# Kernel tuning notes

Measured on AMD Instinct MI355X. Metric: run time of the kernel, lower is better.

The kernel has to match this reference:

```python
import jax, jax.numpy as jnp
import numpy as np

N = 128            # cache entries selected per ray (init arg n)
M = 3 * N          # cache rows
B = 65536          # rays in batch
NUM_SAMPLES = 256  # total samples per ray; inner sampler supplies NUM_SAMPLES - N


def _unit(k, shape):
    v = jax.random.normal(k, shape, dtype=jnp.float32)
    return v / jnp.linalg.norm(v, axis=-1, keepdims=True)


def setup_inputs() -> dict:
    key = jax.random.key(0)
    k0, k1, k2, k3, k4, k5 = jax.random.split(key, 6)
    cache_dirs = _unit(k0, (M, 3))
    cache_mip = jax.random.uniform(k1, (M, 1), dtype=jnp.float32)
    cache_bright = jax.random.uniform(k2, (M, 1), dtype=jnp.float32)
    cache = jnp.concatenate([cache_dirs, cache_mip, cache_bright], axis=1)  # (M,5)
    refdirs = _unit(k3, (B, 3))
    normal = _unit(k4, (B, 3))
    samp_rays = _unit(k5, (B, NUM_SAMPLES - N, 3))
    samp_mipval = jax.random.uniform(jax.random.fold_in(k5, 1), (B, NUM_SAMPLES - N), dtype=jnp.float32)
    return {"cache": cache, "refdirs": refdirs, "normal": normal,
            "samp_rays": samp_rays, "samp_mipval": samp_mipval}


def reference(cache, refdirs, normal, samp_rays, samp_mipval):
    # BrightnessSampler.sample with cache_init=True (n = N cache rays appended).
    cache_dirs = cache[:, :3]      # (M,3)
    cache_mip = cache[:, 3]        # (M,)
    # hemisphere test and directional similarity against every cached ray
    hemi = jnp.einsum('bd,md->bm', normal, cache_dirs)    # (B,M)
    sim = jnp.einsum('bd,md->bm', refdirs, cache_dirs)    # (B,M)
    score = jnp.where(hemi > 0, -sim, jnp.float32(0.0))   # (B,M)
    # torch: inds = argsort(score, dim=1) < n ; boolean-mask gather in original
    # position order. Replicate: keep original positions j where order[b,j] < N.
    order = jnp.argsort(score, axis=1)                    # (B,M)
    mask = order < N
    pos = jnp.where(mask, jnp.arange(M)[None, :], M)
    sel_pos = jnp.sort(pos, axis=1)[:, :N]                # (B,N) ascending original positions
    sel_rays = cache_dirs[sel_pos]                        # (B,N,3)
    sel_mipval = cache_mip[sel_pos]                       # (B,N)
    rays = jnp.concatenate([samp_rays, sel_rays], axis=1)       # (B,NUM_SAMPLES,3)
    mipval = jnp.concatenate([samp_mipval, sel_mipval], axis=1)  # (B,NUM_SAMPLES)
    return rays, mipval
```

## Files before the change

kernel.cpp:

```cpp
#include <hip/hip_runtime.h>

#define NCACHE 384
#define NSEL   128

__device__ __forceinline__ unsigned int sortable_bits(float f) {
    unsigned int u = __float_as_uint(f);
    return (u & 0x80000000u) ? ~u : (u | 0x80000000u);
}

struct __align__(16) u64x2 { unsigned long long x, y; };

__global__ __launch_bounds__(256) void fused_kernel(
    const float*  __restrict__ cache,
    const float*  __restrict__ refdirs,
    const float*  __restrict__ normal,
    const float4* __restrict__ samp_rays4,
    const float4* __restrict__ samp_mip4,
    float* __restrict__ out, int B)
{
#pragma clang fp contract(off)
    __shared__ float sdx[NCACHE], sdy[NCACHE], sdz[NCACHE], smip[NCACHE];
    __shared__ __align__(16) unsigned long long keys[4][NCACHE];
    __shared__ unsigned int bitmap[4][12];

    const int tid  = threadIdx.x;
    const int wave = tid >> 6;
    const int lane = tid & 63;
    const int b    = blockIdx.x * 4 + wave;

    for (int m = tid; m < NCACHE; m += 256) {
        sdx[m]  = cache[m * 5 + 0];
        sdy[m]  = cache[m * 5 + 1];
        sdz[m]  = cache[m * 5 + 2];
        smip[m] = cache[m * 5 + 3];
    }
    if (tid < 48) (&bitmap[0][0])[tid] = 0u;

    const float nx = normal[b * 3 + 0], ny = normal[b * 3 + 1], nz = normal[b * 3 + 2];
    const float rx = refdirs[b * 3 + 0], ry = refdirs[b * 3 + 1], rz = refdirs[b * 3 + 2];

    __syncthreads();

    for (int m = lane; m < NCACHE; m += 64) {
        float dx = sdx[m], dy = sdy[m], dz = sdz[m];
        float hemi = __builtin_fmaf(nz, dz, __builtin_fmaf(ny, dy, nx * dx));
        float sim  = __builtin_fmaf(rz, dz, __builtin_fmaf(ry, dy, rx * dx));
        float val  = (hemi > 0.0f) ? -sim : 0.0f;
        val = val + 0.0f;
        keys[wave][m] = ((unsigned long long)sortable_bits(val) << 32) | (unsigned int)m;
    }
    __syncthreads();

    const unsigned long long k0 = keys[wave][lane];
    const unsigned long long k1 = keys[wave][lane + 64];
    const u64x2* kp = (const u64x2*)&keys[wave][0];
    int r0 = 0, r1 = 0;
#pragma unroll 8
    for (int j = 0; j < NCACHE / 2; ++j) {
        u64x2 kk = kp[j];
        r0 += (kk.x < k0) ? 1 : 0;
        r0 += (kk.y < k0) ? 1 : 0;
        r1 += (kk.x < k1) ? 1 : 0;
        r1 += (kk.y < k1) ? 1 : 0;
    }

    atomicOr(&bitmap[wave][r0 >> 5], 1u << (r0 & 31));
    atomicOr(&bitmap[wave][r1 >> 5], 1u << (r1 & 31));
    __syncthreads();

    float* out_rays = out;
    float* out_mip  = out + (size_t)B * 768;

    {
        const int wi = r0 >> 5;
        int s = __popc(bitmap[wave][wi] & ((1u << (r0 & 31)) - 1u));
        for (int w = 0; w < wi; ++w) s += __popc(bitmap[wave][w]);
        const size_t rb = (size_t)b * 768 + 384 + (size_t)s * 3;
        out_rays[rb + 0] = sdx[r0];
        out_rays[rb + 1] = sdy[r0];
        out_rays[rb + 2] = sdz[r0];
        out_mip[(size_t)b * 256 + 128 + s] = smip[r0];
    }
    {
        const int wi = r1 >> 5;
        int s = __popc(bitmap[wave][wi] & ((1u << (r1 & 31)) - 1u));
        for (int w = 0; w < wi; ++w) s += __popc(bitmap[wave][w]);
        const size_t rb = (size_t)b * 768 + 384 + (size_t)s * 3;
        out_rays[rb + 0] = sdx[r1];
        out_rays[rb + 1] = sdy[r1];
        out_rays[rb + 2] = sdz[r1];
        out_mip[(size_t)b * 256 + 128 + s] = smip[r1];
    }

    float4* out4     = (float4*)out;
    float4* out_mip4 = (float4*)(out + (size_t)B * 768);
    const int b0 = blockIdx.x * 4;
#pragma unroll
    for (int i = tid; i < 512; i += 256) {
        const int bw  = i >> 7;
        const int off = i & 127;
        const int bb  = b0 + bw;
        if (off < 96) {
            out4[(size_t)bb * 192 + off] = samp_rays4[(size_t)bb * 96 + off];
        } else {
            out_mip4[(size_t)bb * 64 + (off - 96)] = samp_mip4[(size_t)bb * 32 + (off - 96)];
        }
    }
}

extern "C" void kernel_launch(void* const* d_in, const int* in_sizes, int n_in,
                              void* d_out, int out_size, void* d_ws, size_t ws_size,
                              hipStream_t stream) {
    const float* cache       = (const float*)d_in[0];
    const float* refdirs     = (const float*)d_in[1];
    const float* normal      = (const float*)d_in[2];
    const float* samp_rays   = (const float*)d_in[3];
    const float* samp_mipval = (const float*)d_in[4];
    float* out = (float*)d_out;

    const int B = in_sizes[1] / 3;

    fused_kernel<<<B / 4, 256, 0, stream>>>(cache, refdirs, normal,
                                            (const float4*)samp_rays,
                                            (const float4*)samp_mipval,
                                            out, B);
}
```

Measured before the change: 208.7 us.

## Compute ranks with wave ballots over register-held keys instead of LDS scan

Keys for all 384 cache entries are now kept in registers (six per lane) rather than written to LDS. Each candidate key is broadcast with readlane, and its rank is counted with six ballots and popcounts across the wave, which removes the LDS key array and one block barrier. The cost is 128 serial broadcast iterations of scalar and ballot work per wave, replacing per-lane streaming compares against 384 LDS keys, plus higher register pressure.

```diff
diff --git a/kernel.cpp b/kernel.cpp
--- a/kernel.cpp
+++ b/kernel.cpp
@@ -1,14 +1,11 @@
 #include <hip/hip_runtime.h>
 
 #define NCACHE 384
-#define NSEL   128
 
 __device__ __forceinline__ unsigned int sortable_bits(float f) {
     unsigned int u = __float_as_uint(f);
     return (u & 0x80000000u) ? ~u : (u | 0x80000000u);
 }
-
-struct __align__(16) u64x2 { unsigned long long x, y; };
 
 __global__ __launch_bounds__(256) void fused_kernel(
     const float*  __restrict__ cache,
@@ -20,7 +17,6 @@
 {
 #pragma clang fp contract(off)
     __shared__ float sdx[NCACHE], sdy[NCACHE], sdz[NCACHE], smip[NCACHE];
-    __shared__ __align__(16) unsigned long long keys[4][NCACHE];
     __shared__ unsigned int bitmap[4][12];
 
     const int tid  = threadIdx.x;
@@ -41,27 +37,35 @@
 
     __syncthreads();
 
-    for (int m = lane; m < NCACHE; m += 64) {
-        float dx = sdx[m], dy = sdy[m], dz = sdz[m];
+    unsigned long long k[6];
+#pragma unroll
+    for (int c = 0; c < 6; ++c) {
+        const int j = c * 64 + lane;
+        float dx = sdx[j], dy = sdy[j], dz = sdz[j];
         float hemi = __builtin_fmaf(nz, dz, __builtin_fmaf(ny, dy, nx * dx));
         float sim  = __builtin_fmaf(rz, dz, __builtin_fmaf(ry, dy, rx * dx));
         float val  = (hemi > 0.0f) ? -sim : 0.0f;
         val = val + 0.0f;
-        keys[wave][m] = ((unsigned long long)sortable_bits(val) << 32) | (unsigned int)m;
+        k[c] = ((unsigned long long)sortable_bits(val) << 32) | (unsigned int)j;
     }
-    __syncthreads();
 
-    const unsigned long long k0 = keys[wave][lane];
-    const unsigned long long k1 = keys[wave][lane + 64];
-    const u64x2* kp = (const u64x2*)&keys[wave][0];
     int r0 = 0, r1 = 0;
-#pragma unroll 8
-    for (int j = 0; j < NCACHE / 2; ++j) {
-        u64x2 kk = kp[j];
-        r0 += (kk.x < k0) ? 1 : 0;
-        r0 += (kk.y < k0) ? 1 : 0;
-        r1 += (kk.x < k1) ? 1 : 0;
-        r1 += (kk.y < k1) ? 1 : 0;
+#pragma unroll
+    for (int c = 0; c < 2; ++c) {
+        const unsigned int klo = (unsigned int)k[c];
+        const unsigned int khi = (unsigned int)(k[c] >> 32);
+#pragma unroll 4
+        for (int l = 0; l < 64; ++l) {
+            const unsigned int mlo = (unsigned int)__builtin_amdgcn_readlane((int)klo, l);
+            const unsigned int mhi = (unsigned int)__builtin_amdgcn_readlane((int)khi, l);
+            const unsigned long long km = ((unsigned long long)mhi << 32) | mlo;
+            int rank = 0;
+#pragma unroll
+            for (int c2 = 0; c2 < 6; ++c2)
+                rank += __popcll(__ballot(k[c2] < km));
+            if (c == 0) r0 = (lane == l) ? rank : r0;
+            else        r1 = (lane == l) ? rank : r1;
+        }
     }
 
     atomicOr(&bitmap[wave][r0 >> 5], 1u << (r0 & 31));
```

New measurement: 242.2 us. 16.0% more time.

## Rank with 32-bit keys in inline asm, half-wave per ray, prefetch copy

Applied to the files above, without the earlier changes.

Each half-wave (32 lanes) now handles one ray instead of a full wave, so a block covers 8 rays. The 64-bit value|index sort keys are replaced by 32-bit keys, and ties are broken by position using lt/le compare selection in hand-written GCN inline asm with carry-add counting. The cache is packed as float4 in LDS, the passthrough sample copy is loaded at kernel start to overlap with compute, and one __syncthreads is dropped. It lowers the ALU and LDS cost of the O(M^2) rank computation, at the cost of fragile inline asm and tie-break logic that must match the reference exactly.

```diff
diff --git a/kernel.cpp b/kernel.cpp
--- a/kernel.cpp
+++ b/kernel.cpp
@@ -1,16 +1,62 @@
 #include <hip/hip_runtime.h>
 
 #define NCACHE 384
-#define NSEL   128
 
 __device__ __forceinline__ unsigned int sortable_bits(float f) {
     unsigned int u = __float_as_uint(f);
     return (u & 0x80000000u) ? ~u : (u | 0x80000000u);
 }
 
-struct __align__(16) u64x2 { unsigned long long x, y; };
 
-__global__ __launch_bounds__(256) void fused_kernel(
+#define JMIX(Q, JOS, O0, O1, O2, O3, KN, RN)                        \
+    "v_cmp_" O0 "_u32 vcc, " Q ", %[k0]\n\t"                        \
+    "v_cmp_" O1 "_u32 %[sc], " Q ", %[k1]\n\t"                      \
+    "v_addc_co_u32 %[r0], vcc, 0, %[r0], vcc\n\t"                   \
+    "v_addc_co_u32 %[r1], %[sc], 0, %[r1], %[sc]\n\t"               \
+    "v_cmp_" O2 "_u32 vcc, " Q ", %[k2]\n\t"                        \
+    "v_cmp_" O3 "_u32 %[sc], " Q ", %[k3]\n\t"                      \
+    "v_addc_co_u32 %[r2], vcc, 0, %[r2], vcc\n\t"                   \
+    "v_addc_co_u32 %[r3], %[sc], 0, %[r3], %[sc]\n\t"               \
+    "v_cmp_eq_u32 vcc, " Q ", %[" KN "]\n\t"                        \
+    "v_bfe_u32 %[t], %[M], " JOS ", 1\n\t"                          \
+    "v_cndmask_b32 %[t], 0, %[t], vcc\n\t"                          \
+    "v_add_u32 %[" RN "], %[t], %[" RN "]\n\t"
+
+#define ITER_MIX(QV, J0, J1, J2, J3, O0, O1, O2, O3, KN, RN)        \
+    do {                                                            \
+        asm(JMIX("%[a]", J0, O0, O1, O2, O3, KN, RN)                \
+            JMIX("%[b]", J1, O0, O1, O2, O3, KN, RN)                \
+            JMIX("%[c]", J2, O0, O1, O2, O3, KN, RN)                \
+            JMIX("%[d]", J3, O0, O1, O2, O3, KN, RN)                \
+            : [r0]"+v"(r0), [r1]"+v"(r1), [r2]"+v"(r2), [r3]"+v"(r3), \
+              [t]"=&v"(t), [sc]"=&s"(sc)                            \
+            : [a]"v"(QV.x), [b]"v"(QV.y), [c]"v"(QV.z), [d]"v"(QV.w), \
+              [k0]"v"(vk0), [k1]"v"(vk1), [k2]"v"(vk2), [k3]"v"(vk3), \
+              [M]"v"(Mmask)                                         \
+            : "vcc");                                               \
+    } while (0)
+
+#define OWN8(KB, O0, O1, O2, O3, KN, RN)                                            \
+    { uint4 q = vq[(KB)*8 + 0]; ITER_MIX(q, "0","1","2","3",     O0,O1,O2,O3,KN,RN); } \
+    { uint4 q = vq[(KB)*8 + 1]; ITER_MIX(q, "4","5","6","7",     O0,O1,O2,O3,KN,RN); } \
+    { uint4 q = vq[(KB)*8 + 2]; ITER_MIX(q, "8","9","10","11",   O0,O1,O2,O3,KN,RN); } \
+    { uint4 q = vq[(KB)*8 + 3]; ITER_MIX(q, "12","13","14","15", O0,O1,O2,O3,KN,RN); } \
+    { uint4 q = vq[(KB)*8 + 4]; ITER_MIX(q, "16","17","18","19", O0,O1,O2,O3,KN,RN); } \
+    { uint4 q = vq[(KB)*8 + 5]; ITER_MIX(q, "20","21","22","23", O0,O1,O2,O3,KN,RN); } \
+    { uint4 q = vq[(KB)*8 + 6]; ITER_MIX(q, "24","25","26","27", O0,O1,O2,O3,KN,RN); } \
+    { uint4 q = vq[(KB)*8 + 7]; ITER_MIX(q, "28","29","30","31", O0,O1,O2,O3,KN,RN); }
+
+#define JLT(Q)                                                      \
+    "v_cmp_lt_u32 vcc, " Q ", %[k0]\n\t"                            \
+    "v_cmp_lt_u32 %[sc], " Q ", %[k1]\n\t"                          \
+    "v_addc_co_u32 %[r0], vcc, 0, %[r0], vcc\n\t"                   \
+    "v_addc_co_u32 %[r1], %[sc], 0, %[r1], %[sc]\n\t"               \
+    "v_cmp_lt_u32 vcc, " Q ", %[k2]\n\t"                            \
+    "v_cmp_lt_u32 %[sc], " Q ", %[k3]\n\t"                          \
+    "v_addc_co_u32 %[r2], vcc, 0, %[r2], vcc\n\t"                   \
+    "v_addc_co_u32 %[r3], %[sc], 0, %[r3], %[sc]\n\t"
+
+__global__ __launch_bounds__(256, 8) void fused_kernel(
     const float*  __restrict__ cache,
     const float*  __restrict__ refdirs,
     const float*  __restrict__ normal,
@@ -19,93 +65,115 @@
     float* __restrict__ out, int B)
 {
 #pragma clang fp contract(off)
-    __shared__ float sdx[NCACHE], sdy[NCACHE], sdz[NCACHE], smip[NCACHE];
-    __shared__ __align__(16) unsigned long long keys[4][NCACHE];
-    __shared__ unsigned int bitmap[4][12];
+    __shared__ __align__(16) float4 scache[NCACHE];
+    __shared__ __align__(16) unsigned int vals[8][NCACHE];
+    __shared__ unsigned int bitmap[8][12];
 
     const int tid  = threadIdx.x;
     const int wave = tid >> 6;
     const int lane = tid & 63;
-    const int b    = blockIdx.x * 4 + wave;
+    const int h    = lane >> 5;
+    const int l5   = lane & 31;
+    const int vidx = wave * 2 + h;
+    const int myb  = blockIdx.x * 8 + vidx;
+
+    const int bbase = blockIdx.x * 8;
+    const int ia = tid, ib = tid + 256, ic = tid + 512, id = tid + 768;
+    const int ba = bbase + (ia >> 7), oa = ia & 127;
+    const int bbb = bbase + (ib >> 7), ob = ib & 127;
+    const int bc = bbase + (ic >> 7), oc = ic & 127;
+    const int bd = bbase + (id >> 7), od = id & 127;
+    const float4 ca = (oa < 96) ? samp_rays4[(size_t)ba * 96 + oa]
+                                : samp_mip4[(size_t)ba * 32 + (oa - 96)];
+    const float4 cb = (ob < 96) ? samp_rays4[(size_t)bbb * 96 + ob]
+                                : samp_mip4[(size_t)bbb * 32 + (ob - 96)];
+    const float4 cc = (oc < 96) ? samp_rays4[(size_t)bc * 96 + oc]
+                                : samp_mip4[(size_t)bc * 32 + (oc - 96)];
+    const float4 cd = (od < 96) ? samp_rays4[(size_t)bd * 96 + od]
+                                : samp_mip4[(size_t)bd * 32 + (od - 96)];
 
     for (int m = tid; m < NCACHE; m += 256) {
-        sdx[m]  = cache[m * 5 + 0];
-        sdy[m]  = cache[m * 5 + 1];
-        sdz[m]  = cache[m * 5 + 2];
-        smip[m] = cache[m * 5 + 3];
+        scache[m] = make_float4(cache[m * 5 + 0], cache[m * 5 + 1],
+                                cache[m * 5 + 2], cache[m * 5 + 3]);
     }
-    if (tid < 48) (&bitmap[0][0])[tid] = 0u;
+    if (tid < 96) (&bitmap[0][0])[tid] = 0u;
 
-    const float nx = normal[b * 3 + 0], ny = normal[b * 3 + 1], nz = normal[b * 3 + 2];
-    const float rx = refdirs[b * 3 + 0], ry = refdirs[b * 3 + 1], rz = refdirs[b * 3 + 2];
+    const float nx = normal[myb * 3 + 0], ny = normal[myb * 3 + 1], nz = normal[myb * 3 + 2];
+    const float rx = refdirs[myb * 3 + 0], ry = refdirs[myb * 3 + 1], rz = refdirs[myb * 3 + 2];
 
     __syncthreads();
 
-    for (int m = lane; m < NCACHE; m += 64) {
-        float dx = sdx[m], dy = sdy[m], dz = sdz[m];
-        float hemi = __builtin_fmaf(nz, dz, __builtin_fmaf(ny, dy, nx * dx));
-        float sim  = __builtin_fmaf(rz, dz, __builtin_fmaf(ry, dy, rx * dx));
+    unsigned int vk0 = 0, vk1 = 0, vk2 = 0, vk3 = 0;
+#pragma unroll
+    for (int c = 0; c < 12; ++c) {
+        const int m = c * 32 + l5;
+        const float4 d = scache[m];
+        float hemi = __builtin_fmaf(nz, d.z, __builtin_fmaf(ny, d.y, nx * d.x));
+        float sim  = __builtin_fmaf(rz, d.z, __builtin_fmaf(ry, d.y, rx * d.x));
         float val  = (hemi > 0.0f) ? -sim : 0.0f;
         val = val + 0.0f;
-        keys[wave][m] = ((unsigned long long)sortable_bits(val) << 32) | (unsigned int)m;
-    }
-    __syncthreads();
-
-    const unsigned long long k0 = keys[wave][lane];
-    const unsigned long long k1 = keys[wave][lane + 64];
-    const u64x2* kp = (const u64x2*)&keys[wave][0];
-    int r0 = 0, r1 = 0;
-#pragma unroll 8
-    for (int j = 0; j < NCACHE / 2; ++j) {
-        u64x2 kk = kp[j];
-        r0 += (kk.x < k0) ? 1 : 0;
-        r0 += (kk.y < k0) ? 1 : 0;
-        r1 += (kk.x < k1) ? 1 : 0;
-        r1 += (kk.y < k1) ? 1 : 0;
+        const unsigned int sv = sortable_bits(val);
+        vals[vidx][m] = sv;
+        if (c == 0) vk0 = sv;
+        if (c == 1) vk1 = sv;
+        if (c == 2) vk2 = sv;
+        if (c == 3) vk3 = sv;
     }
 
-    atomicOr(&bitmap[wave][r0 >> 5], 1u << (r0 & 31));
-    atomicOr(&bitmap[wave][r1 >> 5], 1u << (r1 & 31));
-    __syncthreads();
+    const uint4* vq = (const uint4*)&vals[vidx][0];
+    const unsigned int Mmask = (1u << l5) - 1u;
+    unsigned int r0 = 0, r1 = 0, r2 = 0, r3 = 0;
+    unsigned int t;
+    unsigned long long sc;
+
+    OWN8(0, "lt", "le", "le", "le", "k0", "r0");
+    OWN8(1, "lt", "lt", "le", "le", "k1", "r1");
+    OWN8(2, "lt", "lt", "lt", "le", "k2", "r2");
+    OWN8(3, "lt", "lt", "lt", "lt", "k3", "r3");
+
+#pragma unroll 8
+    for (int i = 32; i < 96; ++i) {
+        const uint4 q = vq[i];
+        asm(JLT("%[a]") JLT("%[b]") JLT("%[c]") JLT("%[d]")
+            : [r0]"+v"(r0), [r1]"+v"(r1), [r2]"+v"(r2), [r3]"+v"(r3),
+              [sc]"=&s"(sc)
+            : [a]"v"(q.x), [b]"v"(q.y), [c]"v"(q.z), [d]"v"(q.w),
+              [k0]"v"(vk0), [k1]"v"(vk1), [k2]"v"(vk2), [k3]"v"(vk3)
+            : "vcc");
+    }
+
+    atomicOr(&bitmap[vidx][r0 >> 5], 1u << (r0 & 31));
+    atomicOr(&bitmap[vidx][r1 >> 5], 1u << (r1 & 31));
+    atomicOr(&bitmap[vidx][r2 >> 5], 1u << (r2 & 31));
+    atomicOr(&bitmap[vidx][r3 >> 5], 1u << (r3 & 31));
 
     float* out_rays = out;
     float* out_mip  = out + (size_t)B * 768;
 
-    {
-        const int wi = r0 >> 5;
-        int s = __popc(bitmap[wave][wi] & ((1u << (r0 & 31)) - 1u));
-        for (int w = 0; w < wi; ++w) s += __popc(bitmap[wave][w]);
-        const size_t rb = (size_t)b * 768 + 384 + (size_t)s * 3;
-        out_rays[rb + 0] = sdx[r0];
-        out_rays[rb + 1] = sdy[r0];
-        out_rays[rb + 2] = sdz[r0];
-        out_mip[(size_t)b * 256 + 128 + s] = smip[r0];
-    }
-    {
-        const int wi = r1 >> 5;
-        int s = __popc(bitmap[wave][wi] & ((1u << (r1 & 31)) - 1u));
-        for (int w = 0; w < wi; ++w) s += __popc(bitmap[wave][w]);
-        const size_t rb = (size_t)b * 768 + 384 + (size_t)s * 3;
-        out_rays[rb + 0] = sdx[r1];
-        out_rays[rb + 1] = sdy[r1];
-        out_rays[rb + 2] = sdz[r1];
-        out_mip[(size_t)b * 256 + 128 + s] = smip[r1];
+#pragma unroll
+    for (int c = 0; c < 4; ++c) {
+        const unsigned int r = (c == 0) ? r0 : (c == 1) ? r1 : (c == 2) ? r2 : r3;
+        const int wi = (int)(r >> 5);
+        int s = __popc(bitmap[vidx][wi] & ((1u << (r & 31)) - 1u));
+        for (int w = 0; w < wi; ++w) s += __popc(bitmap[vidx][w]);
+        const float4 g = scache[r];
+        const size_t rb = (size_t)myb * 768 + 384 + (size_t)s * 3;
+        out_rays[rb + 0] = g.x;
+        out_rays[rb + 1] = g.y;
+        out_rays[rb + 2] = g.z;
+        out_mip[(size_t)myb * 256 + 128 + s] = g.w;
     }
 
     float4* out4     = (float4*)out;
     float4* out_mip4 = (float4*)(out + (size_t)B * 768);
-    const int b0 = blockIdx.x * 4;
-#pragma unroll
-    for (int i = tid; i < 512; i += 256) {
-        const int bw  = i >> 7;
-        const int off = i & 127;
-        const int bb  = b0 + bw;
-        if (off < 96) {
-            out4[(size_t)bb * 192 + off] = samp_rays4[(size_t)bb * 96 + off];
-        } else {
-            out_mip4[(size_t)bb * 64 + (off - 96)] = samp_mip4[(size_t)bb * 32 + (off - 96)];
-        }
-    }
+    if (oa < 96) out4[(size_t)ba * 192 + oa] = ca;
+    else         out_mip4[(size_t)ba * 64 + (oa - 96)] = ca;
+    if (ob < 96) out4[(size_t)bbb * 192 + ob] = cb;
+    else         out_mip4[(size_t)bbb * 64 + (ob - 96)] = cb;
+    if (oc < 96) out4[(size_t)bc * 192 + oc] = cc;
+    else         out_mip4[(size_t)bc * 64 + (oc - 96)] = cc;
+    if (od < 96) out4[(size_t)bd * 192 + od] = cd;
+    else         out_mip4[(size_t)bd * 64 + (od - 96)] = cd;
 }
 
 extern "C" void kernel_launch(void* const* d_in, const int* in_sizes, int n_in,
@@ -120,7 +188,7 @@
 
     const int B = in_sizes[1] / 3;
 
-    fused_kernel<<<B / 4, 256, 0, stream>>>(cache, refdirs, normal,
+    fused_kernel<<<B / 8, 256, 0, stream>>>(cache, refdirs, normal,
                                             (const float4*)samp_rays,
                                             (const float4*)samp_mipval,
                                             out, B);
```

After: 232.0 us. +11.2%, slower.
